# Optimization experiments

Hardware: AMD Instinct MI355X
Metric: run time of the kernel (lower is better)

## Reference

```python
import jax, jax.numpy as jnp
import numpy as np

B, L, DQ = 64, 512, 2048
H, K, DC, DCQ, R = 128, 128, 512, 1536, 64


def setup_inputs() -> dict:
    key = jax.random.key(0)
    ks = jax.random.split(key, 8)
    s = 0.02  # weight scale, kaiming-uniform-ish magnitude
    return {
        "hidden_q": jax.random.normal(ks[0], (B, DQ), jnp.float32),
        "kv_c": jax.random.normal(ks[1], (B, L, DC), jnp.float32),
        "q_proj_w": jax.random.normal(ks[2], (H * K, DQ), jnp.float32) * s,
        "w_kc_q": jax.random.normal(ks[3], (H, K, DCQ), jnp.float32) * s,
        "w_kc_kv": jax.random.normal(ks[4], (H, K, DC), jnp.float32) * s,
        "W_qr": jax.random.normal(ks[5], (H, DCQ, R), jnp.float32) * s / np.sqrt(R).astype(np.float32),
        "W_kr": jax.random.normal(ks[6], (H, DC, R), jnp.float32) * s,
        "out_proj_w": jax.random.normal(ks[7], (DQ, H * K), jnp.float32) * s,
    }


def _rotate_half(x):
    h = x.shape[-1] // 2
    return jnp.concatenate([-x[..., h:], x[..., :h]], axis=-1)


def _rope_tables(seq_len, dim, dtype):
    inv_freq = 1.0 / (10000.0 ** (jnp.arange(0, dim, 2, dtype=dtype) / dim))
    t = jnp.arange(seq_len, dtype=dtype)
    freqs = jnp.einsum('l,d->ld', t, inv_freq)  # [L, dim/2]
    sin = jnp.repeat(jnp.sin(freqs), 2, axis=-1)  # [L, dim]
    cos = jnp.repeat(jnp.cos(freqs), 2, axis=-1)
    return sin, cos


def reference(hidden_q, kv_c, q_proj_w, w_kc_q, w_kc_kv, W_qr, W_kr, out_proj_w):
    Bc, Lc, dc = kv_c.shape
    Hh, Kk, _ = w_kc_q.shape
    # latent query -> per-head q, then low-rank up-projection to d_cq
    q_hk = (hidden_q @ q_proj_w.T).reshape(Bc, Hh, Kk)            # [B,H,K]
    q_big = jnp.einsum('bhk,hkq->bhq', q_hk, w_kc_q)              # [B,H,d_cq]
    # RoPE over compressed kv (d_c-dim rope, half-rotation form)
    sin, cos = _rope_tables(Lc, dc, kv_c.dtype)
    kv = kv_c * cos[None] + _rotate_half(kv_c) * sin[None]        # [B,L,d_c]
    # retrieval-dim projections (NOTE: source einsum 'bld,hdr->bhdr' sums l)
    q_r = jnp.einsum('bhq,hqr->bhr', q_big, W_qr)                 # [B,H,r]
    k_r = jnp.einsum('bld,hdr->bhdr', kv, W_kr)                   # [B,H,d_c,r]
    # fallback attention: scores over the d_c axis, then mix kv rows (L==d_c)
    scores = jnp.einsum('bhr,bhdr->bhd', q_r, k_r)                # [B,H,d_c]
    attn = jax.nn.softmax(scores, axis=-1)
    ctx_c = jnp.einsum('bhj,bjd->bhd', attn, kv)                  # [B,H,d_c]
    # back to per-head latent and output projection
    w_kv_t = jnp.swapaxes(w_kc_kv, 1, 2)                          # [H,d_c,K]
    ctx_lat = jnp.einsum('bhd,hdk->bhk', ctx_c, w_kv_t).reshape(Bc, -1)
    return ctx_lat @ out_proj_w.T                                 # [B,DQ]
```

## Files before the change

kernel.cpp:

```cpp
#include <hip/hip_runtime.h>
#include <hip/hip_bf16.h>
#include <math.h>

#define B_ 64
#define L_ 512
#define DQ_ 2048
#define H_ 128
#define K_ 128
#define DC_ 512
#define DCQ_ 1536
#define R_ 64

#define LOG2_1E4 13.287712379549449f

__global__ void rope_table_kernel(float* __restrict__ sin_t, float* __restrict__ cos_t) {
    int l = blockIdx.x;
    int d = threadIdx.x;
    float if1 = exp2f(-(float)(2 * (d >> 1)) * (LOG2_1E4 / 512.0f));
    float if2 = exp2f(-(float)(2 * ((d + 256) >> 1)) * (LOG2_1E4 / 512.0f));
    float a1 = (float)l * if1, a2 = (float)l * if2;
    float s1, c1, s2, c2;
    sincosf(a1, &s1, &c1);
    sincosf(a2, &s2, &c2);
    sin_t[l * DC_ + d] = s1;       cos_t[l * DC_ + d] = c1;
    sin_t[l * DC_ + d + 256] = s2; cos_t[l * DC_ + d + 256] = c2;
}

__global__ void rope_kernel(const float* __restrict__ kv_c,
                            const float* __restrict__ sin_t, const float* __restrict__ cos_t,
                            float* __restrict__ kv, float* __restrict__ kv_sum) {
    int b = blockIdx.x >> 3;
    int l0 = (blockIdx.x & 7) * 64;
    int d = threadIdx.x;
    const float* base = kv_c + (size_t)b * L_ * DC_;
    float* obase = kv + (size_t)b * L_ * DC_;
    float s_lo = 0.f, s_hi = 0.f;
    for (int l = l0; l < l0 + 64; ++l) {
        float x1 = base[l * DC_ + d];
        float x2 = base[l * DC_ + d + 256];
        float c1 = cos_t[l * DC_ + d],       s1 = sin_t[l * DC_ + d];
        float c2 = cos_t[l * DC_ + d + 256], s2 = sin_t[l * DC_ + d + 256];
        float y1 = fmaf(x1, c1, -x2 * s1);
        float y2 = fmaf(x2, c2,  x1 * s2);
        obase[l * DC_ + d] = y1;
        obase[l * DC_ + d + 256] = y2;
        s_lo += y1; s_hi += y2;
    }
    atomicAdd(&kv_sum[b * DC_ + d], s_lo);
    atomicAdd(&kv_sum[b * DC_ + d + 256], s_hi);
}

template<bool BT>
__global__ __launch_bounds__(256)
void gemm_kernel(const float* __restrict__ A, const float* __restrict__ Bm,
                 float* __restrict__ C,
                 int M, int N, int K,
                 long asb, long bsb, long csb,
                 int lda, int ldb, int ldc,
                 int ksplit)
{
    const int BM = 64, BN = 64, BK = 32;
    __shared__ float As[BK][BM + 4];
    __shared__ float Bs[BK][BN + 4];
    int z = blockIdx.z;
    int mtiles = M / BM;
    int mt = blockIdx.y % mtiles;
    int ks = blockIdx.y / mtiles;
    int n0 = blockIdx.x * BN;
    int m0 = mt * BM;
    int kchunk = K / ksplit;
    int k_begin = ks * kchunk;
    int k_end = k_begin + kchunk;
    const float* Ab = A + asb * z;
    const float* Bb = Bm + bsb * z;
    float* Cb = C + csb * z;
    int tid = threadIdx.x;
    int tn = tid & 15, tm = tid >> 4;

    float acc[4][4] = {};

    for (int k0 = k_begin; k0 < k_end; k0 += BK) {
        {
            int kq = (tid & 7) * 4;
            int m = tid >> 3;
#pragma unroll
            for (int p = 0; p < 2; p++) {
                float4 v = *(const float4*)&Ab[(size_t)(m0 + m + p * 32) * lda + k0 + kq];
                As[kq + 0][m + p * 32] = v.x;
                As[kq + 1][m + p * 32] = v.y;
                As[kq + 2][m + p * 32] = v.z;
                As[kq + 3][m + p * 32] = v.w;
            }
        }
        if (BT) {
            int kq = (tid & 7) * 4;
            int n = tid >> 3;
#pragma unroll
            for (int p = 0; p < 2; p++) {
                float4 v = *(const float4*)&Bb[(size_t)(n0 + n + p * 32) * ldb + k0 + kq];
                Bs[kq + 0][n + p * 32] = v.x;
                Bs[kq + 1][n + p * 32] = v.y;
                Bs[kq + 2][n + p * 32] = v.z;
                Bs[kq + 3][n + p * 32] = v.w;
            }
        } else {
            int nq = (tid & 15) * 4;
            int k = tid >> 4;
#pragma unroll
            for (int p = 0; p < 2; p++) {
                float4 v = *(const float4*)&Bb[(size_t)(k0 + k + p * 16) * ldb + n0 + nq];
                *(float4*)&Bs[k + p * 16][nq] = v;
            }
        }
        __syncthreads();
#pragma unroll
        for (int kk = 0; kk < BK; kk++) {
            float4 a = *(const float4*)&As[kk][tm * 4];
            float4 b = *(const float4*)&Bs[kk][tn * 4];
            float av[4] = {a.x, a.y, a.z, a.w};
            float bv[4] = {b.x, b.y, b.z, b.w};
#pragma unroll
            for (int i = 0; i < 4; i++)
#pragma unroll
                for (int j = 0; j < 4; j++)
                    acc[i][j] = fmaf(av[i], bv[j], acc[i][j]);
        }
        __syncthreads();
    }

    if (ksplit == 1) {
#pragma unroll
        for (int i = 0; i < 4; i++) {
            float4 v = {acc[i][0], acc[i][1], acc[i][2], acc[i][3]};
            *(float4*)&Cb[(size_t)(m0 + tm * 4 + i) * ldc + n0 + tn * 4] = v;
        }
    } else {
#pragma unroll
        for (int i = 0; i < 4; i++)
#pragma unroll
            for (int j = 0; j < 4; j++)
                atomicAdd(&Cb[(size_t)(m0 + tm * 4 + i) * ldc + n0 + tn * 4 + j], acc[i][j]);
    }
}

__global__ void softmax_kernel(const float* __restrict__ s2, const float* __restrict__ kv_sum,
                               float* __restrict__ attn) {
    int b = blockIdx.x >> 7;
    int h = blockIdx.x & 127;
    int d = threadIdx.x;
    const float* srow = s2 + ((size_t)b * H_ + h) * DC_;
    float v1 = srow[d] * kv_sum[b * DC_ + d];
    float v2 = srow[d + 256] * kv_sum[b * DC_ + d + 256];

    __shared__ float red[8];
    int lane = threadIdx.x & 63, wid = threadIdx.x >> 6;

    float m = fmaxf(v1, v2);
    for (int off = 32; off; off >>= 1) m = fmaxf(m, __shfl_down(m, off));
    if (lane == 0) red[wid] = m;
    __syncthreads();
    if (threadIdx.x == 0) {
        float mm = red[0];
        for (int i = 1; i < 4; i++) mm = fmaxf(mm, red[i]);
        red[4] = mm;
    }
    __syncthreads();
    m = red[4];

    float e1 = expf(v1 - m), e2 = expf(v2 - m);
    float s = e1 + e2;
    for (int off = 32; off; off >>= 1) s += __shfl_down(s, off);
    if (lane == 0) red[wid] = s;
    __syncthreads();
    if (threadIdx.x == 0) {
        float ss = 0.f;
        for (int i = 0; i < 4; i++) ss += red[i];
        red[5] = ss;
    }
    __syncthreads();
    float inv = 1.0f / red[5];

    float* arow = attn + ((size_t)b * H_ + h) * DC_;
    arow[d] = e1 * inv;
    arow[d + 256] = e2 * inv;
}

extern "C" void kernel_launch(void* const* d_in, const int* in_sizes, int n_in,
                              void* d_out, int out_size, void* d_ws, size_t ws_size,
                              hipStream_t stream) {
    const float* hidden_q   = (const float*)d_in[0];
    const float* kv_c       = (const float*)d_in[1];
    const float* q_proj_w   = (const float*)d_in[2];
    const float* w_kc_q     = (const float*)d_in[3];
    const float* w_kc_kv    = (const float*)d_in[4];
    const float* W_qr       = (const float*)d_in[5];
    const float* W_kr       = (const float*)d_in[6];
    const float* out_proj_w = (const float*)d_in[7];
    float* out = (float*)d_out;
    float* ws = (float*)d_ws;

    float* sin_t   = ws;
    float* cos_t   = ws + 262144;
    float* kv      = ws + 524288;
    float* kv_sum  = ws + 17301504;
    float* q_hk    = ws + 17334272;
    float* q_big   = ws + 18382848;
    float* q_r     = ws + 30965760;
    float* s2      = ws + 31490048;
    float* ctx_c   = ws + 35684352;
    float* ctx_lat = ws + 39878656;

    hipMemsetAsync(kv_sum,  0, 32768u * 4, stream);
    hipMemsetAsync(q_hk,    0, 1048576u * 4, stream);
    hipMemsetAsync(q_r,     0, 524288u * 4, stream);
    hipMemsetAsync(ctx_lat, 0, 1048576u * 4, stream);
    hipMemsetAsync(out,     0, (size_t)B_ * DQ_ * 4, stream);

    rope_table_kernel<<<512, 256, 0, stream>>>(sin_t, cos_t);
    rope_kernel<<<B_ * 8, 256, 0, stream>>>(kv_c, sin_t, cos_t, kv, kv_sum);

    gemm_kernel<true><<<dim3(16384 / 64, 1 * 2, 1), 256, 0, stream>>>(
        hidden_q, q_proj_w, q_hk, 64, 16384, 2048,
        0, 0, 0, DQ_, DQ_, H_ * K_, 2);

    gemm_kernel<false><<<dim3(1536 / 64, 1, H_), 256, 0, stream>>>(
        q_hk, w_kc_q, q_big, 64, 1536, 128,
        (long)K_, (long)K_ * DCQ_, (long)DCQ_, H_ * K_, DCQ_, H_ * DCQ_, 1);

    gemm_kernel<false><<<dim3(1, 4, H_), 256, 0, stream>>>(
        q_big, W_qr, q_r, 64, 64, 1536,
        (long)DCQ_, (long)DCQ_ * R_, (long)R_, H_ * DCQ_, R_, H_ * R_, 4);

    gemm_kernel<true><<<dim3(512 / 64, 1, H_), 256, 0, stream>>>(
        q_r, W_kr, s2, 64, 512, 64,
        (long)R_, (long)DC_ * R_, (long)DC_, H_ * R_, R_, H_ * DC_, 1);

    softmax_kernel<<<B_ * H_, 256, 0, stream>>>(s2, kv_sum, s2);

    gemm_kernel<false><<<dim3(512 / 64, 2, B_), 256, 0, stream>>>(
        s2, kv, ctx_c, H_, 512, 512,
        (long)H_ * DC_, (long)L_ * DC_, (long)H_ * DC_, DC_, DC_, DC_, 1);

    gemm_kernel<true><<<dim3(128 / 64, 4, H_), 256, 0, stream>>>(
        ctx_c, w_kc_kv, ctx_lat, 64, 128, 512,
        (long)DC_, (long)K_ * DC_, (long)K_, H_ * DC_, DC_, H_ * K_, 4);

    gemm_kernel<true><<<dim3(2048 / 64, 16, 1), 256, 0, stream>>>(
        ctx_lat, out_proj_w, out, 64, 2048, 16384,
        0, 0, 0, H_ * K_, H_ * K_, DQ_, 16);
}
```

Measured before the change: 810.2 us.

## Replace FP32 SIMT GEMMs with bf16 MFMA and fold w_kc_q into W_qr

Swaps the shared-memory FP32 FMA GEMM for a register-only bf16 MFMA kernel that converts operands to bf16 on load, for use on every GEMM stage. It also precomputes W_comb = w_kc_q·W_qr per head, which removes the large q_big intermediate and its two GEMMs. Split-K factors are reduced, which drops the q_r and ctx_lat memsets and cuts atomics. Risks include bf16 precision loss and uncoalesced strided B loads in the non-transposed path without LDS staging.

```diff
diff --git a/kernel.cpp b/kernel.cpp
--- a/kernel.cpp
+++ b/kernel.cpp
@@ -12,6 +12,22 @@
 #define R_ 64
 
 #define LOG2_1E4 13.287712379549449f
+
+typedef __attribute__((ext_vector_type(8))) short bf16x8;
+typedef __attribute__((ext_vector_type(4))) float f32x4;
+
+__device__ __forceinline__ short f2bf(float f) {
+    union { float f; unsigned u; } v; v.f = f;
+    unsigned r = v.u + 0x7fffu + ((v.u >> 16) & 1u);
+    return (short)(r >> 16);
+}
+
+__device__ __forceinline__ bf16x8 cvt8(float4 a, float4 b) {
+    bf16x8 r;
+    r[0] = f2bf(a.x); r[1] = f2bf(a.y); r[2] = f2bf(a.z); r[3] = f2bf(a.w);
+    r[4] = f2bf(b.x); r[5] = f2bf(b.y); r[6] = f2bf(b.z); r[7] = f2bf(b.w);
+    return r;
+}
 
 __global__ void rope_table_kernel(float* __restrict__ sin_t, float* __restrict__ cos_t) {
     int l = blockIdx.x;
@@ -52,94 +68,77 @@
 
 template<bool BT>
 __global__ __launch_bounds__(256)
-void gemm_kernel(const float* __restrict__ A, const float* __restrict__ Bm,
-                 float* __restrict__ C,
-                 int M, int N, int K,
-                 long asb, long bsb, long csb,
-                 int lda, int ldb, int ldc,
-                 int ksplit)
+void gemm_mfma(const float* __restrict__ A, const float* __restrict__ Bm,
+               float* __restrict__ C,
+               int M, int N, int K,
+               long asb, long bsb, long csb,
+               int lda, int ldb, int ldc,
+               int ksplit)
 {
-    const int BM = 64, BN = 64, BK = 32;
-    __shared__ float As[BK][BM + 4];
-    __shared__ float Bs[BK][BN + 4];
     int z = blockIdx.z;
-    int mtiles = M / BM;
+    int mtiles = M >> 6;
     int mt = blockIdx.y % mtiles;
     int ks = blockIdx.y / mtiles;
-    int n0 = blockIdx.x * BN;
-    int m0 = mt * BM;
+    int n0 = blockIdx.x * 64;
+    int m0 = mt * 64;
     int kchunk = K / ksplit;
-    int k_begin = ks * kchunk;
-    int k_end = k_begin + kchunk;
+    int k_begin = ks * kchunk, k_end = k_begin + kchunk;
     const float* Ab = A + asb * z;
     const float* Bb = Bm + bsb * z;
     float* Cb = C + csb * z;
-    int tid = threadIdx.x;
-    int tn = tid & 15, tm = tid >> 4;
-
-    float acc[4][4] = {};
-
-    for (int k0 = k_begin; k0 < k_end; k0 += BK) {
-        {
-            int kq = (tid & 7) * 4;
-            int m = tid >> 3;
-#pragma unroll
-            for (int p = 0; p < 2; p++) {
-                float4 v = *(const float4*)&Ab[(size_t)(m0 + m + p * 32) * lda + k0 + kq];
-                As[kq + 0][m + p * 32] = v.x;
-                As[kq + 1][m + p * 32] = v.y;
-                As[kq + 2][m + p * 32] = v.z;
-                As[kq + 3][m + p * 32] = v.w;
-            }
+
+    int lane = threadIdx.x & 63;
+    int w = threadIdx.x >> 6;
+    int l15 = lane & 15;
+    int kg = lane >> 4;
+    int arow0 = m0 + l15;
+    int nb = n0 + w * 16 + l15;
+
+    f32x4 acc[4] = {{0,0,0,0},{0,0,0,0},{0,0,0,0},{0,0,0,0}};
+
+#pragma unroll 2
+    for (int k0 = k_begin; k0 < k_end; k0 += 32) {
+        int kb = k0 + kg * 8;
+        bf16x8 af[4], bfv;
+#pragma unroll
+        for (int t = 0; t < 4; t++) {
+            const float* p = Ab + (size_t)(arow0 + t * 16) * lda + kb;
+            float4 x = *(const float4*)p;
+            float4 y = *(const float4*)(p + 4);
+            af[t] = cvt8(x, y);
         }
         if (BT) {
-            int kq = (tid & 7) * 4;
-            int n = tid >> 3;
-#pragma unroll
-            for (int p = 0; p < 2; p++) {
-                float4 v = *(const float4*)&Bb[(size_t)(n0 + n + p * 32) * ldb + k0 + kq];
-                Bs[kq + 0][n + p * 32] = v.x;
-                Bs[kq + 1][n + p * 32] = v.y;
-                Bs[kq + 2][n + p * 32] = v.z;
-                Bs[kq + 3][n + p * 32] = v.w;
-            }
+            const float* p = Bb + (size_t)nb * ldb + kb;
+            float4 x = *(const float4*)p;
+            float4 y = *(const float4*)(p + 4);
+            bfv = cvt8(x, y);
         } else {
-            int nq = (tid & 15) * 4;
-            int k = tid >> 4;
-#pragma unroll
-            for (int p = 0; p < 2; p++) {
-                float4 v = *(const float4*)&Bb[(size_t)(k0 + k + p * 16) * ldb + n0 + nq];
-                *(float4*)&Bs[k + p * 16][nq] = v;
-            }
+            const float* p = Bb + (size_t)kb * ldb + nb;
+            float tmp[8];
+#pragma unroll
+            for (int j = 0; j < 8; j++) tmp[j] = p[(size_t)j * ldb];
+#pragma unroll
+            for (int j = 0; j < 8; j++) bfv[j] = f2bf(tmp[j]);
         }
-        __syncthreads();
-#pragma unroll
-        for (int kk = 0; kk < BK; kk++) {
-            float4 a = *(const float4*)&As[kk][tm * 4];
-            float4 b = *(const float4*)&Bs[kk][tn * 4];
-            float av[4] = {a.x, a.y, a.z, a.w};
-            float bv[4] = {b.x, b.y, b.z, b.w};
-#pragma unroll
-            for (int i = 0; i < 4; i++)
-#pragma unroll
-                for (int j = 0; j < 4; j++)
-                    acc[i][j] = fmaf(av[i], bv[j], acc[i][j]);
-        }
-        __syncthreads();
-    }
-
+#pragma unroll
+        for (int t = 0; t < 4; t++)
+            acc[t] = __builtin_amdgcn_mfma_f32_16x16x32_bf16(af[t], bfv, acc[t], 0, 0, 0);
+    }
+
+    int crow0 = m0 + kg * 4;
+    int ccol = n0 + w * 16 + l15;
     if (ksplit == 1) {
 #pragma unroll
-        for (int i = 0; i < 4; i++) {
-            float4 v = {acc[i][0], acc[i][1], acc[i][2], acc[i][3]};
-            *(float4*)&Cb[(size_t)(m0 + tm * 4 + i) * ldc + n0 + tn * 4] = v;
-        }
+        for (int t = 0; t < 4; t++)
+#pragma unroll
+            for (int r = 0; r < 4; r++)
+                Cb[(size_t)(crow0 + t * 16 + r) * ldc + ccol] = acc[t][r];
     } else {
 #pragma unroll
-        for (int i = 0; i < 4; i++)
-#pragma unroll
-            for (int j = 0; j < 4; j++)
-                atomicAdd(&Cb[(size_t)(m0 + tm * 4 + i) * ldc + n0 + tn * 4 + j], acc[i][j]);
+        for (int t = 0; t < 4; t++)
+#pragma unroll
+            for (int r = 0; r < 4; r++)
+                atomicAdd(&Cb[(size_t)(crow0 + t * 16 + r) * ldc + ccol], acc[t][r]);
     }
 }
 
@@ -204,48 +203,51 @@
     float* kv      = ws + 524288;
     float* kv_sum  = ws + 17301504;
     float* q_hk    = ws + 17334272;
-    float* q_big   = ws + 18382848;
-    float* q_r     = ws + 30965760;
-    float* s2      = ws + 31490048;
-    float* ctx_c   = ws + 35684352;
-    float* ctx_lat = ws + 39878656;
-
-    hipMemsetAsync(kv_sum,  0, 32768u * 4, stream);
-    hipMemsetAsync(q_hk,    0, 1048576u * 4, stream);
-    hipMemsetAsync(q_r,     0, 524288u * 4, stream);
-    hipMemsetAsync(ctx_lat, 0, 1048576u * 4, stream);
-    hipMemsetAsync(out,     0, (size_t)B_ * DQ_ * 4, stream);
+    float* W_comb  = ws + 18382848;
+    float* q_r     = ws + 19431424;
+    float* s2      = ws + 19955712;
+    float* ctx_c   = ws + 24150016;
+    float* ctx_lat = ws + 28344320;
+
+    hipMemsetAsync(kv_sum, 0, 32768u * 4, stream);
+    hipMemsetAsync(q_hk,   0, 1048576u * 4, stream);
+    hipMemsetAsync(out,    0, (size_t)B_ * DQ_ * 4, stream);
 
     rope_table_kernel<<<512, 256, 0, stream>>>(sin_t, cos_t);
     rope_kernel<<<B_ * 8, 256, 0, stream>>>(kv_c, sin_t, cos_t, kv, kv_sum);
 
-    gemm_kernel<true><<<dim3(16384 / 64, 1 * 2, 1), 256, 0, stream>>>(
+    gemm_mfma<false><<<dim3(1, 2, H_), 256, 0, stream>>>(
+        w_kc_q, W_qr, W_comb, 128, 64, 1536,
+        (long)K_ * DCQ_, (long)DCQ_ * R_, (long)K_ * R_,
+        DCQ_, R_, R_, 1);
+
+    gemm_mfma<true><<<dim3(256, 2, 1), 256, 0, stream>>>(
         hidden_q, q_proj_w, q_hk, 64, 16384, 2048,
         0, 0, 0, DQ_, DQ_, H_ * K_, 2);
 
-    gemm_kernel<false><<<dim3(1536 / 64, 1, H_), 256, 0, stream>>>(
-        q_hk, w_kc_q, q_big, 64, 1536, 128,
-        (long)K_, (long)K_ * DCQ_, (long)DCQ_, H_ * K_, DCQ_, H_ * DCQ_, 1);
-
-    gemm_kernel<false><<<dim3(1, 4, H_), 256, 0, stream>>>(
-        q_big, W_qr, q_r, 64, 64, 1536,
-        (long)DCQ_, (long)DCQ_ * R_, (long)R_, H_ * DCQ_, R_, H_ * R_, 4);
-
-    gemm_kernel<true><<<dim3(512 / 64, 1, H_), 256, 0, stream>>>(
+    gemm_mfma<false><<<dim3(1, 1, H_), 256, 0, stream>>>(
+        q_hk, W_comb, q_r, 64, 64, 128,
+        (long)K_, (long)K_ * R_, (long)R_,
+        H_ * K_, R_, H_ * R_, 1);
+
+    gemm_mfma<true><<<dim3(8, 1, H_), 256, 0, stream>>>(
         q_r, W_kr, s2, 64, 512, 64,
-        (long)R_, (long)DC_ * R_, (long)DC_, H_ * R_, R_, H_ * DC_, 1);
+        (long)R_, (long)DC_ * R_, (long)DC_,
+        H_ * R_, R_, H_ * DC_, 1);
 
     softmax_kernel<<<B_ * H_, 256, 0, stream>>>(s2, kv_sum, s2);
 
-    gemm_kernel<false><<<dim3(512 / 64, 2, B_), 256, 0, stream>>>(
-        s2, kv, ctx_c, H_, 512, 512,
-        (long)H_ * DC_, (long)L_ * DC_, (long)H_ * DC_, DC_, DC_, DC_, 1);
-
-    gemm_kernel<true><<<dim3(128 / 64, 4, H_), 256, 0, stream>>>(
+    gemm_mfma<false><<<dim3(8, 2, B_), 256, 0, stream>>>(
+        s2, kv, ctx_c, 128, 512, 512,
+        (long)H_ * DC_, (long)L_ * DC_, (long)H_ * DC_,
+        DC_, DC_, DC_, 1);
+
+    gemm_mfma<true><<<dim3(2, 1, H_), 256, 0, stream>>>(
         ctx_c, w_kc_kv, ctx_lat, 64, 128, 512,
-        (long)DC_, (long)K_ * DC_, (long)K_, H_ * DC_, DC_, H_ * K_, 4);
-
-    gemm_kernel<true><<<dim3(2048 / 64, 16, 1), 256, 0, stream>>>(
+        (long)DC_, (long)K_ * DC_, (long)K_,
+        H_ * DC_, DC_, H_ * K_, 1);
+
+    gemm_mfma<true><<<dim3(32, 8, 1), 256, 0, stream>>>(
         ctx_lat, out_proj_w, out, 64, 2048, 16384,
-        0, 0, 0, H_ * K_, H_ * K_, DQ_, 16);
-}
+        0, 0, 0, H_ * K_, H_ * K_, DQ_, 8);
+}
```

Result: faster. 716.2 us (-11.6%).
